# Kernel tuning notes

Measured on AMD Instinct MI355X. Metric: run time of the kernel, lower is better.

The kernel has to match this reference:

```python
import jax, jax.numpy as jnp
import numpy as np

T = 100       # number of landscape sample points (init kwarg T)
K_MAX = 2     # number of landscape layers kept (init kwarg K_max)


def setup_inputs() -> dict:
    key = jax.random.key(0)
    # [B, len_dim, C, N_max, 2]; sort last axis so birth <= death.
    # Padding/invalid pairs would have birth == death and contribute exactly 0,
    # matching the original's zero-row padding of `temp`.
    raw = jax.random.uniform(key, (64, 2, 8, 1024, 2), dtype=jnp.float32)
    diagrams = jnp.sort(raw, axis=-1)
    return {"diagrams": diagrams}


def reference(diagrams):
    # diagrams: [B, D, C, N, 2] with (birth, death) pairs in [0, 1]
    B, D, C, N, _ = diagrams.shape
    birth = diagrams[..., 0:1]                 # [B,D,C,N,1]
    death = diagrams[..., 1:2]                 # [B,D,C,N,1]
    t = jnp.linspace(0.0, 1.0, T, dtype=diagrams.dtype)   # [T]
    # tent function: max(min(t - birth, death - t), 0)  -> [B,D,C,N,T]
    tri = jnp.maximum(jnp.minimum(t - birth, death - t), 0.0)
    # descending sort over persistence pairs, keep top K_MAX layers
    tri_t = jnp.swapaxes(tri, -1, -2)          # [B,D,C,T,N]
    top, _ = jax.lax.top_k(tri_t, K_MAX)       # [B,D,C,T,K]
    # landscape[b, d] = concat over channels along time axis -> [K, C*T]
    pl = jnp.transpose(top, (0, 1, 4, 2, 3))   # [B,D,K,C,T]
    return pl.reshape(B, D, K_MAX, C * T)
```

## Files before the change

kernel.cpp:

```cpp
#include <hip/hip_runtime.h>


typedef _Float16 h2 __attribute__((ext_vector_type(2)));

constexpr int T_PTS = 100;
constexpr int NPTS  = 1024;
constexpr int CCH   = 8;

union U4 { uint4 u; h2 h[4]; };

__global__ __launch_bounds__(128) void pl_topk_kernel(
    const float* __restrict__ diagrams, float* __restrict__ out)
{
    const int g  = blockIdx.x;
    const int c  = g & (CCH - 1);
    const int bd = g >> 3;

    __shared__ alignas(16) h2 mm[NPTS / 2];
    __shared__ alignas(16) h2 hh[NPTS / 2];
    __shared__ float red[2][128][2];

    const float4* src4 = (const float4*)(diagrams + (size_t)g * NPTS * 2);
    for (int i = threadIdx.x; i < NPTS / 2; i += 128) {
        float4 p = src4[i];
        float m0 = 0.5f * (p.x + p.y), h0 = 0.5f * (p.y - p.x);
        float m1 = 0.5f * (p.z + p.w), h1 = 0.5f * (p.w - p.z);
        mm[i] = h2{(_Float16)m0, (_Float16)m1};
        hh[i] = h2{(_Float16)h0, (_Float16)h1};
    }
    __syncthreads();

    const int lane = threadIdx.x & 63;
    const int w    = threadIdx.x >> 6;

    const _Float16 ta = (_Float16)((float)lane * (1.0f / 99.0f));
    const _Float16 tb = (_Float16)((float)(lane + 64) * (1.0f / 99.0f));
    const h2 ta2 = {ta, ta};
    const h2 tb2 = {tb, tb};

    h2 z = {(_Float16)0.0f, (_Float16)0.0f};
    h2 m1a = z, m2a = z, m1b = z, m2b = z;

    const uint4* mm4 = (const uint4*)mm;
    const uint4* hh4 = (const uint4*)hh;
    const int base = w * 64;

    #pragma unroll 4
    for (int i = 0; i < 64; ++i) {
        U4 mu, hu;
        mu.u = mm4[base + i];
        hu.u = hh4[base + i];
        #pragma unroll
        for (int j = 0; j < 4; ++j) {
            h2 mj = mu.h[j], hj = hu.h[j];
            {
                h2 u  = ta2 - mj;
                h2 v  = hj - __builtin_elementwise_abs(u);
                h2 lo = __builtin_elementwise_min(m1a, v);
                m1a = __builtin_elementwise_max(m1a, v);
                m2a = __builtin_elementwise_max(m2a, lo);
            }
            {
                h2 u  = tb2 - mj;
                h2 v  = hj - __builtin_elementwise_abs(u);
                h2 lo = __builtin_elementwise_min(m1b, v);
                m1b = __builtin_elementwise_max(m1b, v);
                m2b = __builtin_elementwise_max(m2b, lo);
            }
        }
    }

    auto reduce2 = [](h2 m1v, h2 m2v, float& hi, float& sec) {
        float p = (float)m1v.x, q = (float)m1v.y;
        float r = (float)m2v.x, s = (float)m2v.y;
        hi  = fmaxf(p, q);
        sec = fmaxf(fminf(p, q), fmaxf(r, s));
    };
    float hia, seca, hib, secb;
    reduce2(m1a, m2a, hia, seca);
    reduce2(m1b, m2b, hib, secb);

    red[w][lane][0]      = hia;  red[w][lane][1]      = seca;
    red[w][lane + 64][0] = hib;  red[w][lane + 64][1] = secb;
    __syncthreads();

    const int t = threadIdx.x;
    if (t < T_PTS) {
        float p = red[0][t][0], r = red[0][t][1];
        float q = red[1][t][0], s = red[1][t][1];
        float top1 = fmaxf(p, q);
        float top2 = fmaxf(fminf(p, q), fmaxf(r, s));
        const size_t basei = (size_t)(bd * 2) * (CCH * T_PTS) + (size_t)c * T_PTS + t;
        out[basei]                 = top1;
        out[basei + CCH * T_PTS]   = top2;
    }
}

extern "C" void kernel_launch(void* const* d_in, const int* in_sizes, int n_in,
                              void* d_out, int out_size, void* d_ws, size_t ws_size,
                              hipStream_t stream) {
    const float* diagrams = (const float*)d_in[0];
    float* out = (float*)d_out;
    pl_topk_kernel<<<1024, 128, 0, stream>>>(diagrams, out);
}
```

Measured before the change: 67.41 us.

## Split persistence points across eight waves and drop midpoint/half-width transform

Raises the block from 128 to 512 threads so each of eight waves scans an eighth of the 1024 pairs, then merges per-wave top-2 results through shared memory. Stores birth and death directly as fp16 and computes the tent as min(t-b, d-t), replacing the midpoint/abs form. This shortens each thread's serial scan and adds parallelism per block, at the cost of a larger cross-wave reduction and more threads per block. Rounding birth and death separately in fp16 may give slightly different values than the old midpoint/half-width encoding.

```diff
diff --git a/kernel.cpp b/kernel.cpp
--- a/kernel.cpp
+++ b/kernel.cpp
@@ -6,27 +6,29 @@
 constexpr int T_PTS = 100;
 constexpr int NPTS  = 1024;
 constexpr int CCH   = 8;
+constexpr int NTHR  = 512;
+constexpr int NWAVES = NTHR / 64;
+constexpr int U4_PER_WAVE = NPTS / NWAVES / 8;
 
 union U4 { uint4 u; h2 h[4]; };
 
-__global__ __launch_bounds__(128) void pl_topk_kernel(
+__global__ __launch_bounds__(NTHR, 8) void pl_topk_kernel(
     const float* __restrict__ diagrams, float* __restrict__ out)
 {
     const int g  = blockIdx.x;
     const int c  = g & (CCH - 1);
     const int bd = g >> 3;
 
-    __shared__ alignas(16) h2 mm[NPTS / 2];
-    __shared__ alignas(16) h2 hh[NPTS / 2];
-    __shared__ float red[2][128][2];
+    __shared__ alignas(16) h2 bb[NPTS / 2];
+    __shared__ alignas(16) h2 dd[NPTS / 2];
+    __shared__ float hi_s[NWAVES][128];
+    __shared__ float se_s[NWAVES][128];
 
-    const float4* src4 = (const float4*)(diagrams + (size_t)g * NPTS * 2);
-    for (int i = threadIdx.x; i < NPTS / 2; i += 128) {
-        float4 p = src4[i];
-        float m0 = 0.5f * (p.x + p.y), h0 = 0.5f * (p.y - p.x);
-        float m1 = 0.5f * (p.z + p.w), h1 = 0.5f * (p.w - p.z);
-        mm[i] = h2{(_Float16)m0, (_Float16)m1};
-        hh[i] = h2{(_Float16)h0, (_Float16)h1};
+    {
+        const float4* src4 = (const float4*)(diagrams + (size_t)g * NPTS * 2);
+        float4 p = src4[threadIdx.x];
+        bb[threadIdx.x] = h2{(_Float16)p.x, (_Float16)p.z};
+        dd[threadIdx.x] = h2{(_Float16)p.y, (_Float16)p.w};
     }
     __syncthreads();
 
@@ -38,33 +40,35 @@
     const h2 ta2 = {ta, ta};
     const h2 tb2 = {tb, tb};
 
-    h2 z = {(_Float16)0.0f, (_Float16)0.0f};
+    const h2 z = {(_Float16)0.0f, (_Float16)0.0f};
     h2 m1a = z, m2a = z, m1b = z, m2b = z;
 
-    const uint4* mm4 = (const uint4*)mm;
-    const uint4* hh4 = (const uint4*)hh;
-    const int base = w * 64;
+    const uint4* bb4 = (const uint4*)bb;
+    const uint4* dd4 = (const uint4*)dd;
+    const int base = w * U4_PER_WAVE;
 
-    #pragma unroll 4
-    for (int i = 0; i < 64; ++i) {
-        U4 mu, hu;
-        mu.u = mm4[base + i];
-        hu.u = hh4[base + i];
+    #pragma unroll 2
+    for (int i = 0; i < U4_PER_WAVE; ++i) {
+        U4 bu, du;
+        bu.u = bb4[base + i];
+        du.u = dd4[base + i];
         #pragma unroll
         for (int j = 0; j < 4; ++j) {
-            h2 mj = mu.h[j], hj = hu.h[j];
+            h2 bj = bu.h[j], dj = du.h[j];
             {
-                h2 u  = ta2 - mj;
-                h2 v  = hj - __builtin_elementwise_abs(u);
-                h2 lo = __builtin_elementwise_min(m1a, v);
-                m1a = __builtin_elementwise_max(m1a, v);
+                h2 u   = ta2 - bj;
+                h2 v   = dj - ta2;
+                h2 tri = __builtin_elementwise_min(u, v);
+                h2 lo  = __builtin_elementwise_min(m1a, tri);
+                m1a = __builtin_elementwise_max(m1a, tri);
                 m2a = __builtin_elementwise_max(m2a, lo);
             }
             {
-                h2 u  = tb2 - mj;
-                h2 v  = hj - __builtin_elementwise_abs(u);
-                h2 lo = __builtin_elementwise_min(m1b, v);
-                m1b = __builtin_elementwise_max(m1b, v);
+                h2 u   = tb2 - bj;
+                h2 v   = dj - tb2;
+                h2 tri = __builtin_elementwise_min(u, v);
+                h2 lo  = __builtin_elementwise_min(m1b, tri);
+                m1b = __builtin_elementwise_max(m1b, tri);
                 m2b = __builtin_elementwise_max(m2b, lo);
             }
         }
@@ -80,19 +84,23 @@
     reduce2(m1a, m2a, hia, seca);
     reduce2(m1b, m2b, hib, secb);
 
-    red[w][lane][0]      = hia;  red[w][lane][1]      = seca;
-    red[w][lane + 64][0] = hib;  red[w][lane + 64][1] = secb;
+    hi_s[w][lane]      = hia;  se_s[w][lane]      = seca;
+    hi_s[w][lane + 64] = hib;  se_s[w][lane + 64] = secb;
     __syncthreads();
 
     const int t = threadIdx.x;
     if (t < T_PTS) {
-        float p = red[0][t][0], r = red[0][t][1];
-        float q = red[1][t][0], s = red[1][t][1];
-        float top1 = fmaxf(p, q);
-        float top2 = fmaxf(fminf(p, q), fmaxf(r, s));
+        float H1 = hi_s[0][t], H2 = se_s[0][t];
+        #pragma unroll
+        for (int wv = 1; wv < NWAVES; ++wv) {
+            float h = hi_s[wv][t], s = se_s[wv][t];
+            float lo = fminf(H1, h);
+            H1 = fmaxf(H1, h);
+            H2 = fmaxf(fmaxf(H2, s), lo);
+        }
         const size_t basei = (size_t)(bd * 2) * (CCH * T_PTS) + (size_t)c * T_PTS + t;
-        out[basei]                 = top1;
-        out[basei + CCH * T_PTS]   = top2;
+        out[basei]               = H1;
+        out[basei + CCH * T_PTS] = H2;
     }
 }
 
@@ -101,5 +109,5 @@
                               hipStream_t stream) {
     const float* diagrams = (const float*)d_in[0];
     float* out = (float*)d_out;
-    pl_topk_kernel<<<1024, 128, 0, stream>>>(diagrams, out);
+    pl_topk_kernel<<<1024, NTHR, 0, stream>>>(diagrams, out);
 }
```

After: 68.74 us. About the same (+2.0%).
